# Optimization experiments

Hardware: AMD Instinct MI355X
Metric: run time of the kernel (lower is better)

Reference implementation:

```python
import jax, jax.numpy as jnp
import numpy as np

S, B, H = 2048, 2, 1024
NH = 16
HD = H // NH
EPS = 1e-5


def _ln(z, w, b):
    m = jnp.mean(z, axis=-1, keepdims=True)
    v = jnp.mean(jnp.square(z - m), axis=-1, keepdims=True)
    return (z - m) * jax.lax.rsqrt(v + EPS) * w + b


def setup_inputs() -> dict:
    key = jax.random.key(0)
    ks = jax.random.split(key, 8)
    std = 0.02
    return {
        "x": jax.random.normal(ks[0], (S, B, H), dtype=jnp.float32),
        "ln1_w": jnp.ones((H,), jnp.float32),
        "ln1_b": jnp.zeros((H,), jnp.float32),
        "w_qkv": jax.random.normal(ks[1], (3 * H, H), jnp.float32) * std,
        "b_qkv": jnp.zeros((3 * H,), jnp.float32),
        "w_proj": jax.random.normal(ks[2], (H, H), jnp.float32) * std,
        "b_proj": jnp.zeros((H,), jnp.float32),
        "ln2_w": jnp.ones((H,), jnp.float32),
        "ln2_b": jnp.zeros((H,), jnp.float32),
        "w_fc1": jax.random.normal(ks[3], (4 * H, H), jnp.float32) * std,
        "b_fc1": jnp.zeros((4 * H,), jnp.float32),
        "w_fc2": jax.random.normal(ks[4], (H, 4 * H), jnp.float32) * std,
        "b_fc2": jnp.zeros((H,), jnp.float32),
    }


def reference(x, ln1_w, ln1_b, w_qkv, b_qkv, w_proj, b_proj,
              ln2_w, ln2_b, w_fc1, b_fc1, w_fc2, b_fc2):
    s, b, h = x.shape
    # --- LayerNormLinear: LN then fused QKV projection ---
    residual = x
    qkv = _ln(x, ln1_w, ln1_b) @ w_qkv.T + b_qkv            # [S, B, 3H]
    # per-head interleaved packing: [S, B, NH, 3*HD] then split on last dim
    qkv = qkv.reshape(s, b, NH, 3 * HD).transpose(1, 2, 0, 3)  # [B, NH, S, 3HD]
    q, k, v = jnp.split(qkv, 3, axis=3)                      # each [B, NH, S, HD]
    # --- naive causal attention with full SxS scores ---
    scores = jnp.einsum("bhsd,bhtd->bhst", q, k) * (HD ** -0.5)
    causal = jnp.triu(jnp.ones((s, s), dtype=bool), k=1)
    scores = jnp.where(causal, -jnp.inf, scores)
    attn = jax.nn.softmax(scores, axis=-1)                   # [B, NH, S, S]
    out = jnp.einsum("bhst,bhtd->bhsd", attn, v)             # [B, NH, S, HD]
    out = out.transpose(0, 2, 1, 3).reshape(b, s, h).transpose(1, 0, 2)  # [S, B, H]
    out = out @ w_proj.T + b_proj
    x = residual + out
    # --- LayerNormMLP: LN -> fc1 -> gelu(tanh) -> fc2, residual ---
    residual = x
    hmid = jax.nn.gelu(_ln(x, ln2_w, ln2_b) @ w_fc1.T + b_fc1, approximate=True)
    x = residual + (hmid @ w_fc2.T + b_fc2)
    return x
```

## Files before the change

kernel.cpp:

```cpp
#include <hip/hip_runtime.h>
#include <math.h>

#define S_LEN 2048
#define B_SZ 2
#define NHEAD 16
#define HDIM 64
#define H_DIM 1024
#define M_ROWS (S_LEN * B_SZ)
#define LN_EPS 1e-5f
#define KSTR 72
#define SCL 0.18033688011112042f

typedef __attribute__((ext_vector_type(4))) float f32x4;
typedef __attribute__((ext_vector_type(8))) short short8;
typedef __attribute__((ext_vector_type(8))) unsigned short u16x8;
typedef __attribute__((ext_vector_type(4))) unsigned short u16x4;
typedef __attribute__((ext_vector_type(2))) unsigned short u16x2;

typedef __attribute__((address_space(3))) unsigned int lds_u32;
typedef const __attribute__((address_space(1))) unsigned int glb_u32;

#define ASM_VMCNT(N) asm volatile("s_waitcnt vmcnt(" #N ")" ::: "memory")

__device__ __forceinline__ float bf2f(unsigned short u) {
    return __uint_as_float(((unsigned int)u) << 16);
}
__device__ __forceinline__ unsigned short f2bf(float f) {
    unsigned int u = __float_as_uint(f);
    return (unsigned short)((u + 0x7fffu + ((u >> 16) & 1u)) >> 16);
}

__global__ __launch_bounds__(256) void cast_all(const float* __restrict__ wqkv,
                                                const float* __restrict__ wproj,
                                                const float* __restrict__ wfc1,
                                                const float* __restrict__ wfc2,
                                                unsigned short* __restrict__ oqkv,
                                                unsigned short* __restrict__ oproj,
                                                unsigned short* __restrict__ ofc1,
                                                unsigned short* __restrict__ ofc2) {
    const int i = blockIdx.x * 256 + threadIdx.x;
    const float* src; unsigned short* dst; int off;
    if (i < 786432)       { src = wqkv;  dst = oqkv;  off = i; }
    else if (i < 1048576) { src = wproj; dst = oproj; off = i - 786432; }
    else if (i < 2097152) { src = wfc1;  dst = ofc1;  off = i - 1048576; }
    else                  { src = wfc2;  dst = ofc2;  off = i - 2097152; }
    f32x4 v = ((const f32x4*)src)[off];
    u16x4 o;
    o.x = f2bf(v.x); o.y = f2bf(v.y); o.z = f2bf(v.z); o.w = f2bf(v.w);
    ((u16x4*)dst)[off] = o;
}

__global__ __launch_bounds__(256) void ln_bf16(const float* __restrict__ x,
                                               const float* __restrict__ w,
                                               const float* __restrict__ b,
                                               unsigned short* __restrict__ y) {
    const int m = blockIdx.x;
    const int tid = threadIdx.x;
    const float* row = x + (size_t)m * H_DIM;

    float4 v = ((const float4*)row)[tid];
    float s  = v.x + v.y + v.z + v.w;
    float ss = v.x * v.x + v.y * v.y + v.z * v.z + v.w * v.w;

    __shared__ float rs[4], rss[4], stats[2];
    const int wave = tid >> 6, lane = tid & 63;
    for (int off = 32; off; off >>= 1) {
        s  += __shfl_down(s, off);
        ss += __shfl_down(ss, off);
    }
    if (lane == 0) { rs[wave] = s; rss[wave] = ss; }
    __syncthreads();
    if (tid == 0) {
        float S = rs[0] + rs[1] + rs[2] + rs[3];
        float SS = rss[0] + rss[1] + rss[2] + rss[3];
        float mean = S * (1.0f / H_DIM);
        float var = SS * (1.0f / H_DIM) - mean * mean;
        stats[0] = mean;
        stats[1] = rsqrtf(var + LN_EPS);
    }
    __syncthreads();
    const float mean = stats[0], inv = stats[1];
    float4 wv = ((const float4*)w)[tid];
    float4 bv = ((const float4*)b)[tid];
    u16x4 o;
    o.x = f2bf((v.x - mean) * inv * wv.x + bv.x);
    o.y = f2bf((v.y - mean) * inv * wv.y + bv.y);
    o.z = f2bf((v.z - mean) * inv * wv.z + bv.z);
    o.w = f2bf((v.w - mean) * inv * wv.w + bv.w);
    ((u16x4*)(y + (size_t)m * H_DIM))[tid] = o;
}

template <int EPI, bool BF_OUT, int TN>
__device__ __forceinline__ void gemm_body(const unsigned short* __restrict__ A,
                                          const unsigned short* __restrict__ B,
                                          const float* __restrict__ bias,
                                          const float* __restrict__ resid,
                                          void* __restrict__ Cout,
                                          int M, int N, int K) {
    constexpr int NJ  = TN / 32;
    constexpr int ANI = 4;
    constexpr int BNI = TN / 32;
    constexpr int NBUF = (TN == 128) ? 2 : 3;
    __shared__ __attribute__((aligned(16))) unsigned short As[NBUF][128 * 64];
    __shared__ __attribute__((aligned(16))) unsigned short Bs[NBUF][TN * 64];

    const int tid = threadIdx.x;
    const int wid = tid >> 6;
    const int ln  = tid & 63;
    const int quad = ln >> 4;
    const int mr   = ln & 15;
    const int wm = (wid >> 1) * 64;
    const int wn = (wid & 1) * (TN / 2);

    const int mb = M >> 7;
    const int stripe = mb >> 3;
    const int xcd = blockIdx.x & 7;
    const int local = blockIdx.x >> 3;
    const int m0 = (xcd * stripe + (local % stripe)) << 7;
    const int n0 = (local / stripe) * TN;

    const int lr = ln >> 3, lc = ln & 7;
    const size_t Kb = (size_t)K * 2;
    const char* gA = (const char*)A + (size_t)(m0 + wid * 32 + lr) * Kb
                     + (size_t)((lc << 4) ^ (lr << 4));
    const int bwr = (TN == 128) ? wid * 32 : wid * 16;
    const char* gB = (const char*)B + (size_t)(n0 + bwr + lr) * Kb
                     + (size_t)((lc << 4) ^ (lr << 4));

    auto stage = [&](int kt, int buf) {
        const char* pa = gA + (size_t)kt * 128;
        unsigned int* la = (unsigned int*)&As[buf][0] + wid * (ANI * 256);
#pragma unroll
        for (int i = 0; i < ANI; i++)
            __builtin_amdgcn_global_load_lds((glb_u32*)(pa + (size_t)i * 8 * Kb),
                                             (lds_u32*)(la + i * 256), 16, 0, 0);
        const char* pb = gB + (size_t)kt * 128;
        unsigned int* lb = (unsigned int*)&Bs[buf][0] + wid * (BNI * 256);
#pragma unroll
        for (int i = 0; i < BNI; i++)
            __builtin_amdgcn_global_load_lds((glb_u32*)(pb + (size_t)i * 8 * Kb),
                                             (lds_u32*)(lb + i * 256), 16, 0, 0);
    };

    const f32x4 zero = {0.f, 0.f, 0.f, 0.f};
    f32x4 acc[4][NJ];
#pragma unroll
    for (int i = 0; i < 4; i++)
#pragma unroll
        for (int j = 0; j < NJ; j++) acc[i][j] = zero;

    const int swz = (mr & 7) << 3;
    auto compute = [&](const unsigned short* As_, const unsigned short* Bs_) {
#pragma unroll
        for (int h = 0; h < 2; h++) {
            short8 af[4], bfr[NJ];
#pragma unroll
            for (int i = 0; i < 4; i++)
                af[i] = *(const short8*)(As_ + (wm + i * 16 + mr) * 64
                                             + ((h * 32 + quad * 8) ^ swz));
#pragma unroll
            for (int j = 0; j < NJ; j++)
                bfr[j] = *(const short8*)(Bs_ + (wn + j * 16 + mr) * 64
                                              + ((h * 32 + quad * 8) ^ swz));
#pragma unroll
            for (int i = 0; i < 4; i++)
#pragma unroll
                for (int j = 0; j < NJ; j++)
                    acc[i][j] = __builtin_amdgcn_mfma_f32_16x16x32_bf16(bfr[j], af[i], acc[i][j], 0, 0, 0);
        }
    };

    const int nt = K >> 6;
    stage(0, 0);
    stage(1, 1);
    if (NBUF == 3) stage(2, 2);

    int cb = 0;
    for (int kt = 0; kt < nt; kt++) {
        if (NBUF == 3) {
            if (kt + 2 < nt)      ASM_VMCNT(12);
            else if (kt + 1 < nt) ASM_VMCNT(6);
            else                  ASM_VMCNT(0);
        } else {
            if (kt + 1 < nt)      ASM_VMCNT(8);
            else                  ASM_VMCNT(0);
        }
        __builtin_amdgcn_s_barrier();
        __builtin_amdgcn_sched_barrier(0);
        compute(&As[cb][0], &Bs[cb][0]);
        __builtin_amdgcn_sched_barrier(0);
        __builtin_amdgcn_s_barrier();
        if (kt + NBUF < nt) stage(kt + NBUF, cb);
        cb = (cb + 1 == NBUF) ? 0 : cb + 1;
    }

    f32x4 bias4[NJ];
#pragma unroll
    for (int j = 0; j < NJ; j++)
        bias4[j] = *(const f32x4*)(bias + n0 + wn + j * 16 + quad * 4);

#pragma unroll
    for (int i = 0; i < 4; i++) {
        const int m = m0 + wm + i * 16 + mr;
#pragma unroll
        for (int j = 0; j < NJ; j++) {
            const int nb = n0 + wn + j * 16 + quad * 4;
            f32x4 v = acc[i][j] + bias4[j];
            if (EPI == 1) v += *(const f32x4*)(resid + (size_t)m * N + nb);
            if (EPI == 2) {
#pragma unroll
                for (int r = 0; r < 4; r++) {
                    const float t = v[r];
                    const float u = t + 0.044715f * t * t * t;
                    const float e = exp2f(2.3022112f * u);
                    v[r] = t - t / (e + 1.0f);
                }
            }
            if (BF_OUT) {
                u16x4 pk;
                pk.x = f2bf(v.x); pk.y = f2bf(v.y); pk.z = f2bf(v.z); pk.w = f2bf(v.w);
                *(u16x4*)((unsigned short*)Cout + (size_t)m * N + nb) = pk;
            } else {
                *(f32x4*)((float*)Cout + (size_t)m * N + nb) = v;
            }
        }
    }
}

__global__ __launch_bounds__(256) void gemm_qkv(const unsigned short* __restrict__ A,
                                                const unsigned short* __restrict__ B,
                                                const float* __restrict__ bias,
                                                void* __restrict__ Cout,
                                                int M, int N, int K) {
    gemm_body<0, true, 128>(A, B, bias, nullptr, Cout, M, N, K);
}
__global__ __launch_bounds__(256) void gemm_proj(const unsigned short* __restrict__ A,
                                                 const unsigned short* __restrict__ B,
                                                 const float* __restrict__ bias,
                                                 const float* __restrict__ resid,
                                                 void* __restrict__ Cout,
                                                 int M, int N, int K) {
    gemm_body<1, false, 64>(A, B, bias, resid, Cout, M, N, K);
}
__global__ __launch_bounds__(256) void gemm_fc1(const unsigned short* __restrict__ A,
                                                const unsigned short* __restrict__ B,
                                                const float* __restrict__ bias,
                                                void* __restrict__ Cout,
                                                int M, int N, int K) {
    gemm_body<2, true, 128>(A, B, bias, nullptr, Cout, M, N, K);
}
__global__ __launch_bounds__(256) void gemm_fc2(const unsigned short* __restrict__ A,
                                                const unsigned short* __restrict__ B,
                                                const float* __restrict__ bias,
                                                const float* __restrict__ resid,
                                                void* __restrict__ Cout,
                                                int M, int N, int K) {
    gemm_body<1, false, 64>(A, B, bias, resid, Cout, M, N, K);
}

__global__ __launch_bounds__(256) void attn_mfma(const unsigned short* __restrict__ qkv,
                                                 unsigned short* __restrict__ out) {
    __shared__ __attribute__((aligned(16))) unsigned short Ks[64 * KSTR];
    __shared__ __attribute__((aligned(16))) unsigned short Vs[64 * KSTR];
    __shared__ __attribute__((aligned(16))) unsigned short Ps[64 * KSTR];

    const int tid = threadIdx.x;
    const int wid = tid >> 6;
    const int ln  = tid & 63;
    const int quad = ln >> 4;
    const int mr   = ln & 15;

    const int id = blockIdx.x;
    const int local = id >> 3;
    const int bh = (id & 7) * 4 + (local >> 4);
    const int pa = local & 15;
    const int b  = bh >> 4;
    const int nh = bh & 15;
    const size_t chan = (size_t)nh * 192;

    const int ksr = tid >> 2, ksc = tid & 3;
    const int vt0 = (tid & 31) * 2, vd0 = (tid >> 5) * 8;

    u16x8 kp0, kp1, vp0, vp1;

#pragma unroll
    for (int half = 0; half < 2; half++) {
        const int qt = half ? (31 - pa) : pa;
        const int qb = qt * 64;

        short8 qf0, qf1;
        {
            const int qrow = qb + wid * 16 + mr;
            const unsigned short* gq = qkv + ((size_t)(qrow * 2 + b)) * 3072 + chan + quad * 8;
            qf0 = *(const short8*)gq;
            qf1 = *(const short8*)(gq + 32);
        }

        const f32x4 zero = {0.f, 0.f, 0.f, 0.f};
        f32x4 o[4];
        float ps = 0.f;
#pragma unroll
        for (int d = 0; d < 4; d++) o[d] = zero;

        {
            const unsigned short* gk = qkv + ((size_t)(ksr * 2 + b)) * 3072 + chan + 64 + ksc * 16;
            kp0 = *(const u16x8*)gk;
            kp1 = *(const u16x8*)(gk + 8);
            const unsigned short* gv = qkv + ((size_t)(vt0 * 2 + b)) * 3072 + chan + 128 + vd0;
            vp0 = *(const u16x8*)gv;
            vp1 = *(const u16x8*)(gv + 6144);
        }

        for (int kt = 0; kt <= qt; kt++) {
            __syncthreads();
            *(u16x8*)(Ks + ksr * KSTR + ksc * 16) = kp0;
            *(u16x8*)(Ks + ksr * KSTR + ksc * 16 + 8) = kp1;
#pragma unroll
            for (int j = 0; j < 8; j++) {
                u16x2 pr; pr.x = vp0[j]; pr.y = vp1[j];
                *(u16x2*)(Vs + (vd0 + j) * KSTR + vt0) = pr;
            }
            if (kt < qt) {
                const int nb = (kt + 1) * 64;
                const unsigned short* gk =
                    qkv + ((size_t)((nb + ksr) * 2 + b)) * 3072 + chan + 64 + ksc * 16;
                kp0 = *(const u16x8*)gk;
                kp1 = *(const u16x8*)(gk + 8);
                const unsigned short* gv =
                    qkv + ((size_t)((nb + vt0) * 2 + b)) * 3072 + chan + 128 + vd0;
                vp0 = *(const u16x8*)gv;
                vp1 = *(const u16x8*)(gv + 6144);
            }
            __syncthreads();

            f32x4 sacc[4];
#pragma unroll
            for (int n = 0; n < 4; n++) {
                sacc[n] = zero;
                const unsigned short* kb = Ks + (n * 16 + mr) * KSTR + quad * 8;
                short8 kfr0 = *(const short8*)kb;
                short8 kfr1 = *(const short8*)(kb + 32);
                sacc[n] = __builtin_amdgcn_mfma_f32_16x16x32_bf16(kfr0, qf0, sacc[n], 0, 0, 0);
                sacc[n] = __builtin_amdgcn_mfma_f32_16x16x32_bf16(kfr1, qf1, sacc[n], 0, 0, 0);
            }
            if (kt == qt) {
#pragma unroll
                for (int n = 0; n < 4; n++)
#pragma unroll
                    for (int r = 0; r < 4; r++)
                        if (n * 16 + quad * 4 + r > wid * 16 + mr) sacc[n][r] = -3.0e38f;
            }

            unsigned short* prow = Ps + (wid * 16 + mr) * KSTR + quad * 4;
#pragma unroll
            for (int n = 0; n < 4; n++) {
                u16x4 pk;
#pragma unroll
                for (int r = 0; r < 4; r++) {
                    const float p = exp2f(fminf(sacc[n][r] * SCL, 80.f));
                    ps += p;
                    pk[r] = (unsigned short)(__float_as_uint(p) >> 16);
                }
                *(u16x4*)(prow + n * 16) = pk;
            }

            {
                const unsigned short* pb = Ps + (wid * 16 + mr) * KSTR + quad * 8;
                short8 pa0 = *(const short8*)pb;
                short8 pa1 = *(const short8*)(pb + 32);
#pragma unroll
                for (int d = 0; d < 4; d++) {
                    const unsigned short* vb = Vs + (d * 16 + mr) * KSTR + quad * 8;
                    short8 vf0 = *(const short8*)vb;
                    short8 vf1 = *(const short8*)(vb + 32);
                    o[d] = __builtin_amdgcn_mfma_f32_16x16x32_bf16(vf0, pa0, o[d], 0, 0, 0);
                    o[d] = __builtin_amdgcn_mfma_f32_16x16x32_bf16(vf1, pa1, o[d], 0, 0, 0);
                }
            }
        }

        ps += __shfl_xor(ps, 16);
        ps += __shfl_xor(ps, 32);
        const float inv = 1.0f / ps;
        const int qrow = qb + wid * 16 + mr;
        unsigned short* po = out + ((size_t)(qrow * 2 + b)) * H_DIM + nh * HDIM;
#pragma unroll
        for (int d = 0; d < 4; d++) {
            u16x4 pk;
#pragma unroll
            for (int r = 0; r < 4; r++) pk[r] = f2bf(o[d][r] * inv);
            *(u16x4*)(po + d * 16 + quad * 4) = pk;
        }
    }
}

extern "C" void kernel_launch(void* const* d_in, const int* in_sizes, int n_in,
                              void* d_out, int out_size, void* d_ws, size_t ws_size,
                              hipStream_t stream) {
    const float* x      = (const float*)d_in[0];
    const float* ln1_w  = (const float*)d_in[1];
    const float* ln1_b  = (const float*)d_in[2];
    const float* w_qkv  = (const float*)d_in[3];
    const float* b_qkv  = (const float*)d_in[4];
    const float* w_proj = (const float*)d_in[5];
    const float* b_proj = (const float*)d_in[6];
    const float* ln2_w  = (const float*)d_in[7];
    const float* ln2_b  = (const float*)d_in[8];
    const float* w_fc1  = (const float*)d_in[9];
    const float* b_fc1  = (const float*)d_in[10];
    const float* w_fc2  = (const float*)d_in[11];
    const float* b_fc2  = (const float*)d_in[12];
    float* out = (float*)d_out;

    char* ws = (char*)d_ws;
    unsigned short* wqkv_bf  = (unsigned short*)(ws);
    unsigned short* wproj_bf = (unsigned short*)(ws + ((size_t)6 << 20));
    unsigned short* wfc1_bf  = (unsigned short*)(ws + ((size_t)8 << 20));
    unsigned short* wfc2_bf  = (unsigned short*)(ws + ((size_t)16 << 20));
    unsigned short* ln_buf   = (unsigned short*)(ws + ((size_t)24 << 20));
    unsigned short* qkv_bf   = (unsigned short*)(ws + ((size_t)32 << 20));
    unsigned short* attn_bf  = (unsigned short*)(ws + ((size_t)56 << 20));
    unsigned short* fc1_bf   = (unsigned short*)(ws + ((size_t)32 << 20));

    cast_all<<<12288, 256, 0, stream>>>(w_qkv, w_proj, w_fc1, w_fc2,
                                        wqkv_bf, wproj_bf, wfc1_bf, wfc2_bf);

    ln_bf16<<<M_ROWS, 256, 0, stream>>>(x, ln1_w, ln1_b, ln_buf);
    gemm_qkv<<<768, 256, 0, stream>>>(ln_buf, wqkv_bf, b_qkv, qkv_bf,
                                      M_ROWS, 3072, 1024);
    attn_mfma<<<512, 256, 0, stream>>>(qkv_bf, attn_bf);
    gemm_proj<<<512, 256, 0, stream>>>(attn_bf, wproj_bf, b_proj, x, out,
                                       M_ROWS, 1024, 1024);
    ln_bf16<<<M_ROWS, 256, 0, stream>>>(out, ln2_w, ln2_b, ln_buf);
    gemm_fc1<<<1024, 256, 0, stream>>>(ln_buf, wfc1_bf, b_fc1, fc1_bf,
                                       M_ROWS, 4096, 1024);
    gemm_fc2<<<512, 256, 0, stream>>>(fc1_bf, wfc2_bf, b_fc2, out, out,
                                      M_ROWS, 1024, 4096);
}
```

Before: 338.6 us.

## Split-K the fc2 GEMM into two partial sums plus a reduction kernel

Replaces the fc2 GEMM (K=4096, 512 blocks) with a split-K version. Two K-halves write fp32 partials to workspace, doubling the grid to 1024 blocks to raise occupancy across CUs. A separate add3 kernel then sums both partials with the residual into the output. This adds 32MB of partial writes and reads plus an extra launch, and falls back to the old kernel when the workspace is too small.

```diff
diff --git a/kernel.cpp b/kernel.cpp
--- a/kernel.cpp
+++ b/kernel.cpp
@@ -258,6 +258,121 @@
     gemm_body<1, false, 64>(A, B, bias, resid, Cout, M, N, K);
 }
 
+__global__ __launch_bounds__(256) void gemm_fc2sk(const unsigned short* __restrict__ A,
+                                                  const unsigned short* __restrict__ B,
+                                                  const float* __restrict__ bias,
+                                                  float* __restrict__ Pout,
+                                                  int M, int N, int K) {
+    constexpr int TN = 64, NJ = 2, ANI = 4, BNI = 2;
+    __shared__ __attribute__((aligned(16))) unsigned short As[2][128 * 64];
+    __shared__ __attribute__((aligned(16))) unsigned short Bs[2][64 * 64];
+
+    const int tid = threadIdx.x;
+    const int wid = tid >> 6;
+    const int ln  = tid & 63;
+    const int quad = ln >> 4;
+    const int mr   = ln & 15;
+    const int wm = (wid >> 1) * 64;
+    const int wn = (wid & 1) * 32;
+
+    const int xcd = blockIdx.x & 7;
+    const int local = blockIdx.x >> 3;
+    const int s = local >> 6;
+    const int rem = local & 63;
+    const int m0 = (xcd * 4 + (rem & 3)) << 7;
+    const int n0 = (rem >> 2) * TN;
+
+    const int Ks = K >> 1;
+    const int lr = ln >> 3, lc = ln & 7;
+    const size_t Kb = (size_t)K * 2;
+    const char* gA = (const char*)A + (size_t)(m0 + wid * 32 + lr) * Kb
+                     + (size_t)s * Ks * 2 + (size_t)((lc << 4) ^ (lr << 4));
+    const char* gB = (const char*)B + (size_t)(n0 + wid * 16 + lr) * Kb
+                     + (size_t)s * Ks * 2 + (size_t)((lc << 4) ^ (lr << 4));
+
+    auto stage = [&](int kt, int buf) {
+        const char* pa = gA + (size_t)kt * 128;
+        unsigned int* la = (unsigned int*)&As[buf][0] + wid * (ANI * 256);
+#pragma unroll
+        for (int i = 0; i < ANI; i++)
+            __builtin_amdgcn_global_load_lds((glb_u32*)(pa + (size_t)i * 8 * Kb),
+                                             (lds_u32*)(la + i * 256), 16, 0, 0);
+        const char* pb = gB + (size_t)kt * 128;
+        unsigned int* lb = (unsigned int*)&Bs[buf][0] + wid * (BNI * 256);
+#pragma unroll
+        for (int i = 0; i < BNI; i++)
+            __builtin_amdgcn_global_load_lds((glb_u32*)(pb + (size_t)i * 8 * Kb),
+                                             (lds_u32*)(lb + i * 256), 16, 0, 0);
+    };
+
+    const f32x4 zero = {0.f, 0.f, 0.f, 0.f};
+    f32x4 acc[4][NJ];
+#pragma unroll
+    for (int i = 0; i < 4; i++)
+#pragma unroll
+        for (int j = 0; j < NJ; j++) acc[i][j] = zero;
+
+    const int swz = (mr & 7) << 3;
+    auto compute = [&](const unsigned short* As_, const unsigned short* Bs_) {
+#pragma unroll
+        for (int h = 0; h < 2; h++) {
+            short8 af[4], bfr[NJ];
+#pragma unroll
+            for (int i = 0; i < 4; i++)
+                af[i] = *(const short8*)(As_ + (wm + i * 16 + mr) * 64
+                                             + ((h * 32 + quad * 8) ^ swz));
+#pragma unroll
+            for (int j = 0; j < NJ; j++)
+                bfr[j] = *(const short8*)(Bs_ + (wn + j * 16 + mr) * 64
+                                              + ((h * 32 + quad * 8) ^ swz));
+#pragma unroll
+            for (int i = 0; i < 4; i++)
+#pragma unroll
+                for (int j = 0; j < NJ; j++)
+                    acc[i][j] = __builtin_amdgcn_mfma_f32_16x16x32_bf16(bfr[j], af[i], acc[i][j], 0, 0, 0);
+        }
+    };
+
+    const int nt = Ks >> 6;
+    stage(0, 0);
+    stage(1, 1);
+    for (int kt = 0; kt < nt; kt++) {
+        if (kt + 1 < nt) ASM_VMCNT(6); else ASM_VMCNT(0);
+        __builtin_amdgcn_s_barrier();
+        __builtin_amdgcn_sched_barrier(0);
+        compute(&As[kt & 1][0], &Bs[kt & 1][0]);
+        __builtin_amdgcn_sched_barrier(0);
+        __builtin_amdgcn_s_barrier();
+        if (kt + 2 < nt) stage(kt + 2, kt & 1);
+    }
+
+    float* P = Pout + (size_t)s * M * N;
+    f32x4 bias4[NJ];
+#pragma unroll
+    for (int j = 0; j < NJ; j++)
+        bias4[j] = (s == 0) ? *(const f32x4*)(bias + n0 + wn + j * 16 + quad * 4) : zero;
+
+#pragma unroll
+    for (int i = 0; i < 4; i++) {
+        const int m = m0 + wm + i * 16 + mr;
+#pragma unroll
+        for (int j = 0; j < NJ; j++) {
+            const int nb = n0 + wn + j * 16 + quad * 4;
+            *(f32x4*)(P + (size_t)m * N + nb) = acc[i][j] + bias4[j];
+        }
+    }
+}
+
+__global__ __launch_bounds__(256) void add3(float* __restrict__ out,
+                                            const float* __restrict__ p0,
+                                            const float* __restrict__ p1,
+                                            int n4) {
+    for (int i = blockIdx.x * 256 + threadIdx.x; i < n4; i += gridDim.x * 256) {
+        f32x4 v = ((const f32x4*)p0)[i] + ((const f32x4*)p1)[i] + ((f32x4*)out)[i];
+        ((f32x4*)out)[i] = v;
+    }
+}
+
 __global__ __launch_bounds__(256) void attn_mfma(const unsigned short* __restrict__ qkv,
                                                  unsigned short* __restrict__ out) {
     __shared__ __attribute__((aligned(16))) unsigned short Ks[64 * KSTR];
@@ -421,6 +536,7 @@
     unsigned short* qkv_bf   = (unsigned short*)(ws + ((size_t)32 << 20));
     unsigned short* attn_bf  = (unsigned short*)(ws + ((size_t)56 << 20));
     unsigned short* fc1_bf   = (unsigned short*)(ws + ((size_t)32 << 20));
+    float* fc2_part = (float*)(ws + ((size_t)64 << 20));
 
     cast_all<<<12288, 256, 0, stream>>>(w_qkv, w_proj, w_fc1, w_fc2,
                                         wqkv_bf, wproj_bf, wfc1_bf, wfc2_bf);
@@ -434,6 +550,14 @@
     ln_bf16<<<M_ROWS, 256, 0, stream>>>(out, ln2_w, ln2_b, ln_buf);
     gemm_fc1<<<1024, 256, 0, stream>>>(ln_buf, wfc1_bf, b_fc1, fc1_bf,
                                        M_ROWS, 4096, 1024);
-    gemm_fc2<<<512, 256, 0, stream>>>(fc1_bf, wfc2_bf, b_fc2, out, out,
-                                      M_ROWS, 1024, 4096);
-}
+    if (ws_size >= ((size_t)96 << 20)) {
+        gemm_fc2sk<<<1024, 256, 0, stream>>>(fc1_bf, wfc2_bf, b_fc2, fc2_part,
+                                             M_ROWS, 1024, 4096);
+        add3<<<2048, 256, 0, stream>>>(out, fc2_part,
+                                       fc2_part + (size_t)M_ROWS * 1024,
+                                       (M_ROWS * 1024) / 4);
+    } else {
+        gemm_fc2<<<512, 256, 0, stream>>>(fc1_bf, wfc2_bf, b_fc2, out, out,
+                                          M_ROWS, 1024, 4096);
+    }
+}
```

After: 353.4 us. 4.4% more time.

## Pre-pack weights into MFMA fragment layout and load B directly to registers

Applied to the files above, without the earlier changes.

The weight cast kernel now writes bf16 weights in a per-lane MFMA fragment order, so each wave can read its B operand straight from global memory into registers with coalesced 16-byte loads. The B tile no longer goes through LDS, which cuts LDS footprint and ds_read traffic. The GEMM main loop is restructured into a two-step ping-pong over A LDS buffers and B register buffers, with adjusted vmcnt waits. The cost is more register pressure and reliance on L2/global latency for B, and the vmcnt counts must match the new mix of load types exactly.

```diff
diff --git a/kernel.cpp b/kernel.cpp
--- a/kernel.cpp
+++ b/kernel.cpp
@@ -30,24 +30,30 @@
     return (unsigned short)((u + 0x7fffu + ((u >> 16) & 1u)) >> 16);
 }
 
-__global__ __launch_bounds__(256) void cast_all(const float* __restrict__ wqkv,
-                                                const float* __restrict__ wproj,
-                                                const float* __restrict__ wfc1,
-                                                const float* __restrict__ wfc2,
-                                                unsigned short* __restrict__ oqkv,
-                                                unsigned short* __restrict__ oproj,
-                                                unsigned short* __restrict__ ofc1,
-                                                unsigned short* __restrict__ ofc2) {
-    const int i = blockIdx.x * 256 + threadIdx.x;
-    const float* src; unsigned short* dst; int off;
-    if (i < 786432)       { src = wqkv;  dst = oqkv;  off = i; }
-    else if (i < 1048576) { src = wproj; dst = oproj; off = i - 786432; }
-    else if (i < 2097152) { src = wfc1;  dst = ofc1;  off = i - 1048576; }
-    else                  { src = wfc2;  dst = ofc2;  off = i - 2097152; }
-    f32x4 v = ((const f32x4*)src)[off];
-    u16x4 o;
-    o.x = f2bf(v.x); o.y = f2bf(v.y); o.z = f2bf(v.z); o.w = f2bf(v.w);
-    ((u16x4*)dst)[off] = o;
+__global__ __launch_bounds__(256) void cast_pack(const float* __restrict__ wqkv,
+                                                 const float* __restrict__ wproj,
+                                                 const float* __restrict__ wfc1,
+                                                 const float* __restrict__ wfc2,
+                                                 unsigned short* __restrict__ oqkv,
+                                                 unsigned short* __restrict__ oproj,
+                                                 unsigned short* __restrict__ ofc1,
+                                                 unsigned short* __restrict__ ofc2) {
+    const int t = blockIdx.x * 256 + threadIdx.x;
+    const int fi = t >> 6, l = t & 63;
+    const float* src; unsigned short* dst; int KC, lf;
+    if (fi < 6144)       { src = wqkv;  dst = oqkv;  KC = 32;  lf = fi; }
+    else if (fi < 8192)  { src = wproj; dst = oproj; KC = 32;  lf = fi - 6144; }
+    else if (fi < 16384) { src = wfc1;  dst = ofc1;  KC = 32;  lf = fi - 8192; }
+    else                 { src = wfc2;  dst = ofc2;  KC = 128; lf = fi - 16384; }
+    const int K = KC * 32;
+    const int nt = lf / KC, kc = lf - nt * KC;
+    const float* p = src + (size_t)(nt * 16 + (l & 15)) * K + kc * 32 + (l >> 4) * 8;
+    f32x4 a = *(const f32x4*)p;
+    f32x4 b = *(const f32x4*)(p + 4);
+    u16x8 o;
+    o[0] = f2bf(a.x); o[1] = f2bf(a.y); o[2] = f2bf(a.z); o[3] = f2bf(a.w);
+    o[4] = f2bf(b.x); o[5] = f2bf(b.y); o[6] = f2bf(b.z); o[7] = f2bf(b.w);
+    *(u16x8*)(dst + ((size_t)lf * 64 + l) * 8) = o;
 }
 
 __global__ __launch_bounds__(256) void ln_bf16(const float* __restrict__ x,
@@ -92,17 +98,13 @@
 
 template <int EPI, bool BF_OUT, int TN>
 __device__ __forceinline__ void gemm_body(const unsigned short* __restrict__ A,
-                                          const unsigned short* __restrict__ B,
+                                          const unsigned short* __restrict__ Bp,
                                           const float* __restrict__ bias,
                                           const float* __restrict__ resid,
                                           void* __restrict__ Cout,
                                           int M, int N, int K) {
-    constexpr int NJ  = TN / 32;
-    constexpr int ANI = 4;
-    constexpr int BNI = TN / 32;
-    constexpr int NBUF = (TN == 128) ? 2 : 3;
-    __shared__ __attribute__((aligned(16))) unsigned short As[NBUF][128 * 64];
-    __shared__ __attribute__((aligned(16))) unsigned short Bs[NBUF][TN * 64];
+    constexpr int NJ = TN / 32;
+    __shared__ __attribute__((aligned(16))) unsigned short As[2][128 * 64];
 
     const int tid = threadIdx.x;
     const int wid = tid >> 6;
@@ -123,23 +125,25 @@
     const size_t Kb = (size_t)K * 2;
     const char* gA = (const char*)A + (size_t)(m0 + wid * 32 + lr) * Kb
                      + (size_t)((lc << 4) ^ (lr << 4));
-    const int bwr = (TN == 128) ? wid * 32 : wid * 16;
-    const char* gB = (const char*)B + (size_t)(n0 + bwr + lr) * Kb
-                     + (size_t)((lc << 4) ^ (lr << 4));
 
     auto stage = [&](int kt, int buf) {
         const char* pa = gA + (size_t)kt * 128;
-        unsigned int* la = (unsigned int*)&As[buf][0] + wid * (ANI * 256);
-#pragma unroll
-        for (int i = 0; i < ANI; i++)
+        unsigned int* la = (unsigned int*)&As[buf][0] + wid * (4 * 256);
+#pragma unroll
+        for (int i = 0; i < 4; i++)
             __builtin_amdgcn_global_load_lds((glb_u32*)(pa + (size_t)i * 8 * Kb),
                                              (lds_u32*)(la + i * 256), 16, 0, 0);
-        const char* pb = gB + (size_t)kt * 128;
-        unsigned int* lb = (unsigned int*)&Bs[buf][0] + wid * (BNI * 256);
-#pragma unroll
-        for (int i = 0; i < BNI; i++)
-            __builtin_amdgcn_global_load_lds((glb_u32*)(pb + (size_t)i * 8 * Kb),
-                                             (lds_u32*)(lb + i * 256), 16, 0, 0);
+    };
+
+    const int KC = K >> 5;
+    const unsigned short* gBp = Bp + ((size_t)((n0 + wn) >> 4) * KC * 64 + ln) * 8;
+    auto loadB = [&](int kt, u16x8 (&bb)[NJ][2]) {
+#pragma unroll
+        for (int j = 0; j < NJ; j++)
+#pragma unroll
+            for (int h = 0; h < 2; h++)
+                bb[j][h] = *(const u16x8*)(gBp
+                              + ((size_t)j * KC + (kt * 2 + h)) * 64 * 8);
     };
 
     const f32x4 zero = {0.f, 0.f, 0.f, 0.f};
@@ -150,48 +154,54 @@
         for (int j = 0; j < NJ; j++) acc[i][j] = zero;
 
     const int swz = (mr & 7) << 3;
-    auto compute = [&](const unsigned short* As_, const unsigned short* Bs_) {
+    auto compute = [&](const unsigned short* As_, u16x8 (&bc)[NJ][2]) {
 #pragma unroll
         for (int h = 0; h < 2; h++) {
-            short8 af[4], bfr[NJ];
+            short8 af[4];
 #pragma unroll
             for (int i = 0; i < 4; i++)
                 af[i] = *(const short8*)(As_ + (wm + i * 16 + mr) * 64
                                              + ((h * 32 + quad * 8) ^ swz));
 #pragma unroll
-            for (int j = 0; j < NJ; j++)
-                bfr[j] = *(const short8*)(Bs_ + (wn + j * 16 + mr) * 64
-                                              + ((h * 32 + quad * 8) ^ swz));
-#pragma unroll
             for (int i = 0; i < 4; i++)
 #pragma unroll
                 for (int j = 0; j < NJ; j++)
-                    acc[i][j] = __builtin_amdgcn_mfma_f32_16x16x32_bf16(bfr[j], af[i], acc[i][j], 0, 0, 0);
+                    acc[i][j] = __builtin_amdgcn_mfma_f32_16x16x32_bf16(
+                        (short8)bc[j][h], af[i], acc[i][j], 0, 0, 0);
         }
     };
 
+    u16x8 bA[NJ][2], bB[NJ][2];
     const int nt = K >> 6;
     stage(0, 0);
     stage(1, 1);
-    if (NBUF == 3) stage(2, 2);
-
-    int cb = 0;
-    for (int kt = 0; kt < nt; kt++) {
-        if (NBUF == 3) {
-            if (kt + 2 < nt)      ASM_VMCNT(12);
-            else if (kt + 1 < nt) ASM_VMCNT(6);
-            else                  ASM_VMCNT(0);
+    loadB(0, bA);
+
+    for (int kt = 0; kt < nt; kt += 2) {
+        if (kt + 1 < nt) {
+            if (TN == 128) ASM_VMCNT(12); else ASM_VMCNT(8);
         } else {
-            if (kt + 1 < nt)      ASM_VMCNT(8);
-            else                  ASM_VMCNT(0);
+            if (TN == 128) ASM_VMCNT(8);  else ASM_VMCNT(4);
         }
         __builtin_amdgcn_s_barrier();
+        if (kt + 1 < nt) loadB(kt + 1, bB);
         __builtin_amdgcn_sched_barrier(0);
-        compute(&As[cb][0], &Bs[cb][0]);
+        compute(&As[0][0], bA);
         __builtin_amdgcn_sched_barrier(0);
         __builtin_amdgcn_s_barrier();
-        if (kt + NBUF < nt) stage(kt + NBUF, cb);
-        cb = (cb + 1 == NBUF) ? 0 : cb + 1;
+        if (kt + 2 < nt) stage(kt + 2, 0);
+        if (kt + 2 < nt) {
+            if (TN == 128) ASM_VMCNT(12); else ASM_VMCNT(8);
+        } else {
+            if (TN == 128) ASM_VMCNT(8);  else ASM_VMCNT(4);
+        }
+        __builtin_amdgcn_s_barrier();
+        if (kt + 2 < nt) loadB(kt + 2, bA);
+        __builtin_amdgcn_sched_barrier(0);
+        compute(&As[1][0], bB);
+        __builtin_amdgcn_sched_barrier(0);
+        __builtin_amdgcn_s_barrier();
+        if (kt + 3 < nt) stage(kt + 3, 1);
     }
 
     f32x4 bias4[NJ];
@@ -422,7 +432,7 @@
     unsigned short* attn_bf  = (unsigned short*)(ws + ((size_t)56 << 20));
     unsigned short* fc1_bf   = (unsigned short*)(ws + ((size_t)32 << 20));
 
-    cast_all<<<12288, 256, 0, stream>>>(w_qkv, w_proj, w_fc1, w_fc2,
+    cast_pack<<<6144, 256, 0, stream>>>(w_qkv, w_proj, w_fc1, w_fc2,
                                         wqkv_bf, wproj_bf, wfc1_bf, wfc2_bf);
 
     ln_bf16<<<M_ROWS, 256, 0, stream>>>(x, ln1_w, ln1_b, ln_buf);
```

New measurement: 331.5 us. -2.1%, faster.
